# Optimization experiments

Measured on AMD Instinct MI355X. Metric: run time of the kernel, lower is better.

Reference implementation:

```python
import jax, jax.numpy as jnp
import numpy as np

B, L, A, D, H = 128, 48, 16, 256, 128
NEG = 1e10


def l2norm(v, eps=1e-8):
    return v / (jnp.sqrt(jnp.sum(v * v, axis=-1, keepdims=True)) + eps)


def setup_inputs():
    key = jax.random.key(0)
    ks = jax.random.split(key, 6)
    x = jax.random.normal(ks[0], (B, L, A, D), jnp.float32)
    lengths = jax.random.randint(ks[1], (B,), 8, L + 1)
    lengths = lengths.at[0].set(L)  # forward assumes lengths.max() == L
    audio_masks = (jax.random.uniform(ks[2], (B, L, A, 1)) < 0.7).astype(jnp.float32)
    audio_masks = audio_masks.at[..., 0, :].set(1.0)  # at least one valid frame per word
    w_sem = jax.random.normal(ks[3], (D, D), jnp.float32) * 0.05   # Linear(D,D,bias=False).weight
    w1 = jax.random.normal(ks[4], (H, 2 * D), jnp.float32) * 0.05  # Linear(2D,H).weight
    b1 = jnp.zeros((H,), jnp.float32)
    w2 = jax.random.normal(ks[5], (1, H), jnp.float32) * 0.05      # Linear(H,1,bias=False).weight
    return {"x": x, "lengths": lengths, "audio_masks": audio_masks,
            "w_sem": w_sem, "w1": w1, "b1": b1, "w2": w2}


def _merge(arr, cv, idx):
    """update_with_mask with fixed-length arrays: new[j]=arr[j] (j<idx), cv (j==idx), arr[j+1] (j>idx).
    Trailing garbage slot is masked downstream by length masks."""
    shift = jnp.concatenate([arr[:, 1:], arr[:, -1:]], axis=1)
    extra = (1,) * (arr.ndim - 2)
    j = jnp.arange(arr.shape[1]).reshape((1, -1) + extra)
    ib = idx.reshape((-1, 1) + extra)
    return jnp.where(j < ib, arr, jnp.where(j == ib, jnp.expand_dims(cv, 1), shift))


def _forward(x, lengths, audio_masks, w_sem, w1, b1, w2):
    Bq, Lq = x.shape[0], x.shape[1]
    S = Lq - 1  # max_select_cnt (lengths.max() == Lq)
    # masked max over audio frames: [B,L,D]
    sem0 = jnp.max(jnp.einsum('blad,ed->blae', x, w_sem) - NEG * (1.0 - audio_masks), axis=-2)
    word_mask = (jnp.arange(Lq)[None, :] < lengths[:, None]).astype(x.dtype)
    out_word = sem0 * word_mask[..., None]
    pos = jnp.arange(Lq, dtype=jnp.int32)
    bounds0 = jnp.broadcast_to(pos, (Bq, Lq))
    posm1 = jnp.arange(Lq - 1)

    def gat(a, k):  # gather along axis 1 at per-batch index
        return jnp.take_along_axis(a, k.reshape((-1, 1) + (1,) * (a.ndim - 2)), axis=1)[:, 0]

    def step(carry, i):
        syn, sem, lb, rb = carry
        valid = jnp.clip(lengths - 1 - i, 0)               # merges still allowed per sentence
        masked = (posm1[None, :] >= valid[:, None]).astype(x.dtype)
        undone = (valid > 0).astype(x.dtype)[:, None]
        feats = jnp.concatenate([l2norm(syn[:, 1:]), l2norm(syn[:, :-1])], axis=-1)  # [B,L-1,2D]
        h = jax.nn.relu(jnp.einsum('bld,hd->blh', feats, w1) + b1)
        logits = jnp.einsum('blh,oh->blo', h, w2)[..., 0] - NEG * masked
        probs = jax.nn.softmax(logits, axis=1)
        idx = jnp.argmax(probs, axis=1).astype(jnp.int32)  # volatile=True (greedy) path
        tp = jnp.take_along_axis(probs, idx[:, None], axis=1)[:, 0]
        s_l, s_r = gat(sem, idx), gat(sem, idx + 1)
        feat = l2norm(s_l + s_r)
        spans = jnp.stack([gat(lb, idx), gat(rb, idx + 1)], axis=1)  # [B,2]
        syn_c = l2norm(gat(syn, idx) + gat(syn, idx + 1))
        carry = (_merge(syn, syn_c, idx), _merge(sem, feat, idx),
                 _merge(lb, spans[:, 0], idx), _merge(rb, spans[:, 1], idx))
        outs = (feat * undone, l2norm(s_l) * undone, l2norm(s_r) * undone, idx, tp, spans)
        return carry, outs

    _, (features, lefts, rights, tree_idx, tree_probs, span_bounds) = jax.lax.scan(
        step, (sem0, sem0, bounds0, bounds0), jnp.arange(S))
    return features, lefts, rights, out_word, tree_idx, tree_probs, span_bounds


def reference(x, lengths, audio_masks, w_sem, w1, b1, w2):
    return _forward(x, lengths, audio_masks, w_sem, w1, b1, w2)
```

## Files before the change

kernel.cpp:

```cpp
#include <hip/hip_runtime.h>
#include <math.h>

#define NEGC 1e10f
#define EPSF 1e-8f

#define NB 128
#define NL 48
#define NA 16
#define ND 256
#define NH 128
#define NS 47
#define PB_STRIDE (NL*ND)

#define WS_WT   0
#define WS_INVN 65536
#define WS_LOG  (65536+6144)
#define WS_PHYS (65536+12288)

#define O_FEAT  0
#define O_LEFT  1540096
#define O_RIGHT 3080192
#define O_WORD  4620288
#define O_TIDX  6193152
#define O_TP    6199168
#define O_SPAN  6205184

__device__ __forceinline__ void ldsbar() {
  asm volatile("s_waitcnt lgkmcnt(0)" ::: "memory");
  __builtin_amdgcn_s_barrier();
  __builtin_amdgcn_sched_barrier(0);
}

__global__ __launch_bounds__(256) void k_transpose(const float* __restrict__ w_sem,
                                                   float* __restrict__ ws) {
  int blk = blockIdx.x, t = threadIdx.x;
  ws[WS_WT + blk*256 + t] = w_sem[t*256 + blk];
}

__global__ __launch_bounds__(128) void k_sem0(const float* __restrict__ x,
                                              const int* __restrict__ lengths,
                                              const float* __restrict__ amask,
                                              float* __restrict__ ws,
                                              float* __restrict__ out) {
  __shared__ float xs[2*NA*128];
  __shared__ float pen[2*NA];
  int bl0 = blockIdx.x * 2;
  int t = threadIdx.x;
  int wv = t >> 6;
  int c = t & 63;
  int bl = bl0 + wv;
  int b = bl / NL, l = bl - b*NL;
  int l0 = bl0 % NL;
  int lenB = lengths[bl0 / NL];
  int e0 = c*4;

  if (l0 >= lenB) {
    float4 z = make_float4(0.f, 0.f, 0.f, 0.f);
    *(float4*)(ws + WS_PHYS + (size_t)b*PB_STRIDE + l*ND + e0) = z;
    *(float4*)(out + O_WORD + (size_t)bl*ND + e0) = z;
    if (c == 0) ws[WS_INVN + bl] = 1.0f / (sqrtf(0.f) + EPSF);
    return;
  }
  bool live  = (l < lenB);
  bool live1 = (l0 + 1 < lenB);

  if (t < 2*NA) pen[t] = -NEGC * (1.0f - amask[(size_t)(bl0 + (t >> 4))*NA + (t & 15)]);
  float4* xs4 = (float4*)xs;
  const float* wt = ws + WS_WT;
  float acc[NA][4];
#pragma unroll
  for (int a = 0; a < NA; ++a) { acc[a][0]=0.f; acc[a][1]=0.f; acc[a][2]=0.f; acc[a][3]=0.f; }
  bool va[NA];

  for (int p = 0; p < 2; ++p) {
    if (p) __syncthreads();
#pragma unroll
    for (int r = 0; r < 8; ++r) {
      int f = t + 128*r;
      int tile = f >> 9, rem = f & 511;
      int a = rem >> 5, dq = rem & 31;
      if (tile == 0 || live1) {
        const float4* xg4 = (const float4*)(x + (size_t)(bl0 + tile)*(NA*ND));
        xs4[f] = xg4[a*64 + p*32 + dq];
      }
    }
    __syncthreads();
    if (p == 0) {
#pragma unroll
      for (int a = 0; a < NA; ++a) va[a] = live && (pen[wv*NA + a] == 0.0f);
    }
    if (live) {
      for (int d0 = 0; d0 < 128; d0 += 4) {
        const float* wrow = wt + (size_t)(p*128 + d0)*ND + e0;
        float4 wr0 = *(const float4*)(wrow);
        float4 wr1 = *(const float4*)(wrow + ND);
        float4 wr2 = *(const float4*)(wrow + 2*ND);
        float4 wr3 = *(const float4*)(wrow + 3*ND);
#pragma unroll
        for (int a = 0; a < NA; ++a) {
          if (va[a]) {
            float4 xa = xs4[wv*512 + a*32 + (d0 >> 2)];
            acc[a][0] = fmaf(xa.x, wr0.x, acc[a][0]);
            acc[a][1] = fmaf(xa.x, wr0.y, acc[a][1]);
            acc[a][2] = fmaf(xa.x, wr0.z, acc[a][2]);
            acc[a][3] = fmaf(xa.x, wr0.w, acc[a][3]);
            acc[a][0] = fmaf(xa.y, wr1.x, acc[a][0]);
            acc[a][1] = fmaf(xa.y, wr1.y, acc[a][1]);
            acc[a][2] = fmaf(xa.y, wr1.z, acc[a][2]);
            acc[a][3] = fmaf(xa.y, wr1.w, acc[a][3]);
            acc[a][0] = fmaf(xa.z, wr2.x, acc[a][0]);
            acc[a][1] = fmaf(xa.z, wr2.y, acc[a][1]);
            acc[a][2] = fmaf(xa.z, wr2.z, acc[a][2]);
            acc[a][3] = fmaf(xa.z, wr2.w, acc[a][3]);
            acc[a][0] = fmaf(xa.w, wr3.x, acc[a][0]);
            acc[a][1] = fmaf(xa.w, wr3.y, acc[a][1]);
            acc[a][2] = fmaf(xa.w, wr3.z, acc[a][2]);
            acc[a][3] = fmaf(xa.w, wr3.w, acc[a][3]);
          }
        }
      }
    }
  }
  float m0 = -INFINITY, m1 = -INFINITY, m2 = -INFINITY, m3 = -INFINITY;
#pragma unroll
  for (int a = 0; a < NA; ++a) {
    if (va[a]) {
      m0 = fmaxf(m0, acc[a][0]);
      m1 = fmaxf(m1, acc[a][1]);
      m2 = fmaxf(m2, acc[a][2]);
      m3 = fmaxf(m3, acc[a][3]);
    }
  }
  if (!live) { m0 = 0.f; m1 = 0.f; m2 = 0.f; m3 = 0.f; }
  float* prow = ws + WS_PHYS + (size_t)b*PB_STRIDE + l*ND;
  *(float4*)(prow + e0) = make_float4(m0, m1, m2, m3);
  float wm = live ? 1.0f : 0.0f;
  *(float4*)(out + O_WORD + (size_t)bl*ND + e0) = make_float4(m0*wm, m1*wm, m2*wm, m3*wm);
  float s2 = m0*m0 + m1*m1 + m2*m2 + m3*m3;
#pragma unroll
  for (int off = 32; off; off >>= 1) s2 += __shfl_down(s2, off);
  if (c == 0) ws[WS_INVN + bl] = 1.0f / (sqrtf(s2) + EPSF);
}

__global__ __launch_bounds__(512, 1) void k_prelogits(float* __restrict__ ws,
                                                      const int* __restrict__ lengths,
                                                      const float* __restrict__ w1g,
                                                      const float* __restrict__ b1g,
                                                      const float* __restrict__ w2g) {
  __shared__ float rows[25*ND];
  __shared__ float part[4*8*NH];
  __shared__ float invl[25];
  __shared__ float b1s[NH];
  __shared__ float w2s[NH];
  int bid = blockIdx.x;
  int b = bid >> 1, h = bid & 1;
  int p0 = h*24;
  int np = h ? 23 : 24;
  int nrows = h ? 24 : 25;
  int t = threadIdx.x;
  int lane = t & 63, wv = t >> 6;
  int j = t & 127, q = t >> 7;

  int lenB = lengths[b];
  int npl = lenB - 1 - p0;
  if (npl > np) npl = np;
  if (npl <= 0) return;

  float w1f[128];
  {
    const float4* wsrc = (const float4*)(w1g + (size_t)j*512 + q*128);
#pragma unroll
    for (int kk = 0; kk < 32; ++kk) {
      float4 v = wsrc[kk];
      w1f[4*kk+0] = v.x; w1f[4*kk+1] = v.y; w1f[4*kk+2] = v.z; w1f[4*kk+3] = v.w;
    }
  }
#pragma unroll
  for (int kk = 0; kk < 32; ++kk)
    asm volatile("" : "+v"(w1f[4*kk+0]), "+v"(w1f[4*kk+1]), "+v"(w1f[4*kk+2]), "+v"(w1f[4*kk+3]));

  if (t < NH) { b1s[t] = b1g[t]; w2s[t] = w2g[t]; }
  if (t < nrows) invl[t] = ws[WS_INVN + b*48 + p0 + t];
  {
    const float4* pg4 = (const float4*)(ws + WS_PHYS + (size_t)b*PB_STRIDE);
    float4* rows4 = (float4*)rows;
    int n4 = nrows * 64;
    for (int u = t; u < n4; u += 512) rows4[u] = pg4[p0*64 + u];
  }
  __syncthreads();

  for (int ct = 0; ct < 3; ++ct) {
    if (ct*8 >= npl) break;
#pragma unroll
    for (int c = 0; c < 8; ++c) {
      int pp = ct*8 + c;
      if (pp < npl) {
        int rloc = (q < 2) ? pp + 1 : pp;
        const float4* rp4 = (const float4*)(rows + rloc*ND + (q & 1)*128);
        float ax = 0.f, ay = 0.f, az = 0.f, aw = 0.f;
#pragma unroll
        for (int kk = 0; kk < 32; ++kk) {
          float4 rv = rp4[kk];
          ax = fmaf(w1f[4*kk+0], rv.x, ax);
          ay = fmaf(w1f[4*kk+1], rv.y, ay);
          az = fmaf(w1f[4*kk+2], rv.z, az);
          aw = fmaf(w1f[4*kk+3], rv.w, aw);
        }
        part[(q*8 + c)*NH + j] = (ax + ay) + (az + aw);
      }
    }
    __syncthreads();
    int pp = ct*8 + wv;
    if (pp < npl) {
      float inR = invl[pp + 1], inL = invl[pp];
      float pr0 = part[(0*8+wv)*NH + lane]      + part[(1*8+wv)*NH + lane];
      float pl0 = part[(2*8+wv)*NH + lane]      + part[(3*8+wv)*NH + lane];
      float pr1 = part[(0*8+wv)*NH + lane + 64] + part[(1*8+wv)*NH + lane + 64];
      float pl1 = part[(2*8+wv)*NH + lane + 64] + part[(3*8+wv)*NH + lane + 64];
      float h0 = fmaf(inR, pr0, fmaf(inL, pl0, b1s[lane]));
      float h1 = fmaf(inR, pr1, fmaf(inL, pl1, b1s[lane + 64]));
      h0 = fmaxf(h0, 0.f); h1 = fmaxf(h1, 0.f);
      float v = w2s[lane]*h0 + w2s[lane + 64]*h1;
#pragma unroll
      for (int off = 32; off; off >>= 1) v += __shfl_down(v, off);
      if (lane == 0) ws[WS_LOG + b*48 + p0 + pp] = v;
    }
    __syncthreads();
  }
}

__global__ __launch_bounds__(1024, 1) void k_tree(const int* __restrict__ lengths,
                                                  float* __restrict__ ws,
                                                  const float* __restrict__ w1g,
                                                  const float* __restrict__ b1g,
                                                  const float* __restrict__ w2g,
                                                  float* __restrict__ out) {
  __shared__ float rows[NL*ND];
  __shared__ float part[16*NH];
  __shared__ float logits[48];
  __shared__ int physIdx[48];
  __shared__ int lbA[48];
  __shared__ int rbA[48];
  __shared__ float invn[48];
  __shared__ float b1s[NH];
  __shared__ float w2s[NH];
  __shared__ float red[8];
  __shared__ int s_idx, s_rL;
  __shared__ float s_tp, s_max;

  int b = blockIdx.x;
  int t = threadIdx.x;
  int lane = t & 63, wv = t >> 6;
  int j = t & 127, s8 = t >> 7;
  int len = lengths[b];

  float w1f[64];
  {
    const float4* wsrc = (const float4*)(w1g + (size_t)j*512 + s8*64);
#pragma unroll
    for (int kk = 0; kk < 16; ++kk) {
      float4 v = wsrc[kk];
      w1f[4*kk+0] = v.x; w1f[4*kk+1] = v.y; w1f[4*kk+2] = v.z; w1f[4*kk+3] = v.w;
    }
  }
#pragma unroll
  for (int kk = 0; kk < 16; ++kk)
    asm volatile("" : "+v"(w1f[4*kk+0]), "+v"(w1f[4*kk+1]), "+v"(w1f[4*kk+2]), "+v"(w1f[4*kk+3]));

  if (t < NH) { b1s[t] = b1g[t]; w2s[t] = w2g[t]; }
  if (t < 48) { physIdx[t] = t; lbA[t] = t; rbA[t] = t; invn[t] = ws[WS_INVN + b*48 + t]; }
  if (t < 47) logits[t] = ws[WS_LOG + b*48 + t];
  {
    const float4* pg4 = (const float4*)(ws + WS_PHYS + (size_t)b*PB_STRIDE);
    float4* rows4 = (float4*)rows;
    for (int u = t; u < NL*64; u += 1024) rows4[u] = pg4[u];
  }
  __syncthreads();

  auto gemv_pos = [&](int pos, int slot) {
    int r = (s8 < 4) ? physIdx[pos + 1] : physIdx[pos];
    const float4* rp4 = (const float4*)(rows + r*ND + (s8 & 3)*64);
    float ax = 0.f, ay = 0.f, az = 0.f, aw = 0.f;
#pragma unroll
    for (int kk = 0; kk < 16; ++kk) {
      float4 rv = rp4[kk];
      ax = fmaf(w1f[4*kk+0], rv.x, ax);
      ay = fmaf(w1f[4*kk+1], rv.y, ay);
      az = fmaf(w1f[4*kk+2], rv.z, az);
      aw = fmaf(w1f[4*kk+3], rv.w, aw);
    }
    part[(s8*2 + slot)*NH + j] = (ax + ay) + (az + aw);
  };

  int pidx = -1;
  for (int i = 0; i < NS; ++i) {
    int valid = len - 1 - i; if (valid < 0) valid = 0;
    if (i > 0 && t == 0)
      invn[s_rL] = 1.0f / (sqrtf(red[4]+red[5]+red[6]+red[7]) + EPSF);
    if (valid >= 2) {
      if (i > 0) {
        int pos0 = -1, pos1 = -1, np = 0;
        if (pidx > 0) { pos0 = pidx - 1; np = 1; }
        if (pidx <= valid - 1) { if (np) pos1 = pidx; else pos0 = pidx; ++np; }
        gemv_pos(pos0, 0);
        if (np > 1) gemv_pos(pos1, 1);
        ldsbar();
        if (wv < np) {
          int p = (wv == 0) ? pos0 : pos1;
          int rR = physIdx[p + 1], rLL = physIdx[p];
          float inR = invn[rR], inL = invn[rLL];
          float pr0 = (part[(0*2+wv)*NH + lane]      + part[(1*2+wv)*NH + lane])
                    + (part[(2*2+wv)*NH + lane]      + part[(3*2+wv)*NH + lane]);
          float pl0 = (part[(4*2+wv)*NH + lane]      + part[(5*2+wv)*NH + lane])
                    + (part[(6*2+wv)*NH + lane]      + part[(7*2+wv)*NH + lane]);
          float pr1 = (part[(0*2+wv)*NH + lane + 64] + part[(1*2+wv)*NH + lane + 64])
                    + (part[(2*2+wv)*NH + lane + 64] + part[(3*2+wv)*NH + lane + 64]);
          float pl1 = (part[(4*2+wv)*NH + lane + 64] + part[(5*2+wv)*NH + lane + 64])
                    + (part[(6*2+wv)*NH + lane + 64] + part[(7*2+wv)*NH + lane + 64]);
          float h0 = fmaf(inR, pr0, fmaf(inL, pl0, b1s[lane]));
          float h1 = fmaf(inR, pr1, fmaf(inL, pl1, b1s[lane + 64]));
          h0 = fmaxf(h0, 0.f); h1 = fmaxf(h1, 0.f);
          float v = w2s[lane]*h0 + w2s[lane + 64]*h1;
#pragma unroll
          for (int off = 32; off; off >>= 1) v += __shfl_down(v, off);
          if (lane == 0) logits[p] = v;
        }
        ldsbar();
      }
      if (wv == 0) {
        float v = (lane < valid) ? logits[lane] : -INFINITY;
        int bi = lane;
#pragma unroll
        for (int off = 32; off; off >>= 1) {
          float ov = __shfl_down(v, off);
          int  oi = __shfl_down(bi, off);
          if (ov > v || (ov == v && oi < bi)) { v = ov; bi = oi; }
        }
        if (lane == 0) { s_idx = bi; s_max = v; }
      }
    } else {
      if (t == 0) { s_idx = 0; s_tp = (valid == 1) ? 1.0f : (1.0f/47.0f); }
    }
    ldsbar();
    int idx = s_idx;
    int rL = 0, rR = 0; float slv = 0.f, srv = 0.f, inL = 0.f, inR = 0.f, sumv = 0.f;
    if (t < ND) {
      rL = physIdx[idx]; rR = physIdx[idx + 1];
      slv = rows[rL*ND + t]; srv = rows[rR*ND + t];
      inL = invn[rL]; inR = invn[rR];
      sumv = slv + srv;
      float q2 = sumv * sumv;
#pragma unroll
      for (int off = 32; off; off >>= 1) q2 += __shfl_down(q2, off);
      if (lane == 0) red[wv] = q2;
    }
    int sp0 = 0, sp1 = 0;
    if (t == 0) { s_rL = rL; sp0 = lbA[idx]; sp1 = rbA[idx + 1]; }
    if (wv == 4 && valid >= 2) {
      float ee = (lane < valid) ? expf(logits[lane] - s_max) : 0.f;
#pragma unroll
      for (int off = 32; off; off >>= 1) ee += __shfl_down(ee, off);
      if (lane == 0) s_tp = 1.0f / ee;
    }
    int tt = t - 320;
    int pv = 0, lv = 0, rv_ = 0; float gv = 0.f;
    if (wv == 5 && tt < 47) { pv = physIdx[tt+1]; lv = lbA[tt+1]; rv_ = rbA[tt+1]; gv = logits[tt+1]; }
    ldsbar();
    float undone = valid > 0 ? 1.0f : 0.0f;
    if (t < ND) {
      float invns = 1.0f / (sqrtf(red[0]+red[1]+red[2]+red[3]) + EPSF);
      float featv = sumv * invns;
      int ob = (i*NB + b)*ND + t;
      out[O_FEAT  + ob] = featv * undone;
      out[O_LEFT  + ob] = slv * inL * undone;
      out[O_RIGHT + ob] = srv * inR * undone;
      rows[rL*ND + t] = featv;
      float q3 = featv * featv;
#pragma unroll
      for (int off = 32; off; off >>= 1) q3 += __shfl_down(q3, off);
      if (lane == 0) red[4 + wv] = q3;
    }
    if (t == 0) {
      out[O_TIDX + i*NB + b] = (float)idx;
      out[O_TP   + i*NB + b] = s_tp;
      out[O_SPAN + (i*NB + b)*2 + 0] = (float)sp0;
      out[O_SPAN + (i*NB + b)*2 + 1] = (float)sp1;
    }
    if (wv == 5 && tt < 47) {
      if (tt > idx) { physIdx[tt] = pv; lbA[tt] = lv; logits[tt] = gv; }
      if (tt >= idx) rbA[tt] = rv_;
    }
    ldsbar();
    pidx = idx;
  }
}

extern "C" void kernel_launch(void* const* d_in, const int* in_sizes, int n_in,
                              void* d_out, int out_size, void* d_ws, size_t ws_size,
                              hipStream_t stream) {
  const float* x      = (const float*)d_in[0];
  const int*   lengths= (const int*)  d_in[1];
  const float* amask  = (const float*)d_in[2];
  const float* w_sem  = (const float*)d_in[3];
  const float* w1     = (const float*)d_in[4];
  const float* b1     = (const float*)d_in[5];
  const float* w2     = (const float*)d_in[6];
  float* out = (float*)d_out;
  float* ws  = (float*)d_ws;

  k_transpose<<<dim3(256), dim3(256), 0, stream>>>(w_sem, ws);
  k_sem0<<<dim3(NB*NL/2), dim3(128), 0, stream>>>(x, lengths, amask, ws, out);
  k_prelogits<<<dim3(256), dim3(512), 0, stream>>>(ws, lengths, w1, b1, w2);
  k_tree<<<dim3(NB), dim3(1024), 0, stream>>>(lengths, ws, w1, b1, w2, out);
}
```

Before: 326.9 us.

## Prefetch weight rows in sem0 and fuse logit finish with argmax in one wave

In the sem0 projection kernel, the next four transposed-weight rows are loaded into registers with inline asm while the current rows feed the FMAs, and a launch-bounds occupancy hint is added. The goal is to hide global load latency in the inner loop. In the sequential tree loop, wave 0 now computes both updated logits and runs the argmax directly from registers. This removes one LDS barrier and a round trip through shared memory per step. The trade-offs are extra register pressure from double-buffered weights and less wave parallelism in the logit computation.

Result: slower. 373.2 us (+14.2%).

```diff
diff --git a/kernel.cpp b/kernel.cpp
--- a/kernel.cpp
+++ b/kernel.cpp
@@ -31,17 +31,19 @@
   __builtin_amdgcn_sched_barrier(0);
 }
 
+#define GLOAD4(dst, addr) asm volatile("global_load_dwordx4 %0, %1, off" : "=v"(dst) : "v"(addr))
+
 __global__ __launch_bounds__(256) void k_transpose(const float* __restrict__ w_sem,
                                                    float* __restrict__ ws) {
   int blk = blockIdx.x, t = threadIdx.x;
   ws[WS_WT + blk*256 + t] = w_sem[t*256 + blk];
 }
 
-__global__ __launch_bounds__(128) void k_sem0(const float* __restrict__ x,
-                                              const int* __restrict__ lengths,
-                                              const float* __restrict__ amask,
-                                              float* __restrict__ ws,
-                                              float* __restrict__ out) {
+__global__ __launch_bounds__(128, 4) void k_sem0(const float* __restrict__ x,
+                                                 const int* __restrict__ lengths,
+                                                 const float* __restrict__ amask,
+                                                 float* __restrict__ ws,
+                                                 float* __restrict__ out) {
   __shared__ float xs[2*NA*128];
   __shared__ float pen[2*NA];
   int bl0 = blockIdx.x * 2;
@@ -72,6 +74,15 @@
   for (int a = 0; a < NA; ++a) { acc[a][0]=0.f; acc[a][1]=0.f; acc[a][2]=0.f; acc[a][3]=0.f; }
   bool va[NA];
 
+  float4 cw0, cw1, cw2, cw3, nw0, nw1, nw2, nw3;
+  {
+    const float* wr = wt + e0;
+    cw0 = *(const float4*)(wr);
+    cw1 = *(const float4*)(wr + ND);
+    cw2 = *(const float4*)(wr + 2*ND);
+    cw3 = *(const float4*)(wr + 3*ND);
+  }
+
   for (int p = 0; p < 2; ++p) {
     if (p) __syncthreads();
 #pragma unroll
@@ -91,32 +102,41 @@
     }
     if (live) {
       for (int d0 = 0; d0 < 128; d0 += 4) {
-        const float* wrow = wt + (size_t)(p*128 + d0)*ND + e0;
-        float4 wr0 = *(const float4*)(wrow);
-        float4 wr1 = *(const float4*)(wrow + ND);
-        float4 wr2 = *(const float4*)(wrow + 2*ND);
-        float4 wr3 = *(const float4*)(wrow + 3*ND);
+        int g = p*128 + d0;
+        bool pf = (g < 252);
+        if (pf) {
+          const float* wr = wt + (size_t)(g + 4)*ND + e0;
+          GLOAD4(nw0, wr);
+          GLOAD4(nw1, wr + ND);
+          GLOAD4(nw2, wr + 2*ND);
+          GLOAD4(nw3, wr + 3*ND);
+        }
 #pragma unroll
         for (int a = 0; a < NA; ++a) {
           if (va[a]) {
             float4 xa = xs4[wv*512 + a*32 + (d0 >> 2)];
-            acc[a][0] = fmaf(xa.x, wr0.x, acc[a][0]);
-            acc[a][1] = fmaf(xa.x, wr0.y, acc[a][1]);
-            acc[a][2] = fmaf(xa.x, wr0.z, acc[a][2]);
-            acc[a][3] = fmaf(xa.x, wr0.w, acc[a][3]);
-            acc[a][0] = fmaf(xa.y, wr1.x, acc[a][0]);
-            acc[a][1] = fmaf(xa.y, wr1.y, acc[a][1]);
-            acc[a][2] = fmaf(xa.y, wr1.z, acc[a][2]);
-            acc[a][3] = fmaf(xa.y, wr1.w, acc[a][3]);
-            acc[a][0] = fmaf(xa.z, wr2.x, acc[a][0]);
-            acc[a][1] = fmaf(xa.z, wr2.y, acc[a][1]);
-            acc[a][2] = fmaf(xa.z, wr2.z, acc[a][2]);
-            acc[a][3] = fmaf(xa.z, wr2.w, acc[a][3]);
-            acc[a][0] = fmaf(xa.w, wr3.x, acc[a][0]);
-            acc[a][1] = fmaf(xa.w, wr3.y, acc[a][1]);
-            acc[a][2] = fmaf(xa.w, wr3.z, acc[a][2]);
-            acc[a][3] = fmaf(xa.w, wr3.w, acc[a][3]);
+            acc[a][0] = fmaf(xa.x, cw0.x, acc[a][0]);
+            acc[a][1] = fmaf(xa.x, cw0.y, acc[a][1]);
+            acc[a][2] = fmaf(xa.x, cw0.z, acc[a][2]);
+            acc[a][3] = fmaf(xa.x, cw0.w, acc[a][3]);
+            acc[a][0] = fmaf(xa.y, cw1.x, acc[a][0]);
+            acc[a][1] = fmaf(xa.y, cw1.y, acc[a][1]);
+            acc[a][2] = fmaf(xa.y, cw1.z, acc[a][2]);
+            acc[a][3] = fmaf(xa.y, cw1.w, acc[a][3]);
+            acc[a][0] = fmaf(xa.z, cw2.x, acc[a][0]);
+            acc[a][1] = fmaf(xa.z, cw2.y, acc[a][1]);
+            acc[a][2] = fmaf(xa.z, cw2.z, acc[a][2]);
+            acc[a][3] = fmaf(xa.z, cw2.w, acc[a][3]);
+            acc[a][0] = fmaf(xa.w, cw3.x, acc[a][0]);
+            acc[a][1] = fmaf(xa.w, cw3.y, acc[a][1]);
+            acc[a][2] = fmaf(xa.w, cw3.z, acc[a][2]);
+            acc[a][3] = fmaf(xa.w, cw3.w, acc[a][3]);
           }
+        }
+        if (pf) {
+          asm volatile("s_waitcnt vmcnt(0)" ::: "memory");
+          __builtin_amdgcn_sched_barrier(0);
+          cw0 = nw0; cw1 = nw1; cw2 = nw2; cw3 = nw3;
         }
       }
     }
@@ -305,38 +325,68 @@
         gemv_pos(pos0, 0);
         if (np > 1) gemv_pos(pos1, 1);
         ldsbar();
-        if (wv < np) {
-          int p = (wv == 0) ? pos0 : pos1;
-          int rR = physIdx[p + 1], rLL = physIdx[p];
-          float inR = invn[rR], inL = invn[rLL];
-          float pr0 = (part[(0*2+wv)*NH + lane]      + part[(1*2+wv)*NH + lane])
-                    + (part[(2*2+wv)*NH + lane]      + part[(3*2+wv)*NH + lane]);
-          float pl0 = (part[(4*2+wv)*NH + lane]      + part[(5*2+wv)*NH + lane])
-                    + (part[(6*2+wv)*NH + lane]      + part[(7*2+wv)*NH + lane]);
-          float pr1 = (part[(0*2+wv)*NH + lane + 64] + part[(1*2+wv)*NH + lane + 64])
-                    + (part[(2*2+wv)*NH + lane + 64] + part[(3*2+wv)*NH + lane + 64]);
-          float pl1 = (part[(4*2+wv)*NH + lane + 64] + part[(5*2+wv)*NH + lane + 64])
-                    + (part[(6*2+wv)*NH + lane + 64] + part[(7*2+wv)*NH + lane + 64]);
-          float h0 = fmaf(inR, pr0, fmaf(inL, pl0, b1s[lane]));
-          float h1 = fmaf(inR, pr1, fmaf(inL, pl1, b1s[lane + 64]));
+        if (wv == 0) {
+          float inR0 = invn[physIdx[pos0 + 1]], inL0 = invn[physIdx[pos0]];
+          float pr0 = (part[(0*2+0)*NH + lane]      + part[(1*2+0)*NH + lane])
+                    + (part[(2*2+0)*NH + lane]      + part[(3*2+0)*NH + lane]);
+          float pl0 = (part[(4*2+0)*NH + lane]      + part[(5*2+0)*NH + lane])
+                    + (part[(6*2+0)*NH + lane]      + part[(7*2+0)*NH + lane]);
+          float pr1 = (part[(0*2+0)*NH + lane + 64] + part[(1*2+0)*NH + lane + 64])
+                    + (part[(2*2+0)*NH + lane + 64] + part[(3*2+0)*NH + lane + 64]);
+          float pl1 = (part[(4*2+0)*NH + lane + 64] + part[(5*2+0)*NH + lane + 64])
+                    + (part[(6*2+0)*NH + lane + 64] + part[(7*2+0)*NH + lane + 64]);
+          float h0 = fmaf(inR0, pr0, fmaf(inL0, pl0, b1s[lane]));
+          float h1 = fmaf(inR0, pr1, fmaf(inL0, pl1, b1s[lane + 64]));
           h0 = fmaxf(h0, 0.f); h1 = fmaxf(h1, 0.f);
-          float v = w2s[lane]*h0 + w2s[lane + 64]*h1;
-#pragma unroll
-          for (int off = 32; off; off >>= 1) v += __shfl_down(v, off);
-          if (lane == 0) logits[p] = v;
-        }
-        ldsbar();
-      }
-      if (wv == 0) {
-        float v = (lane < valid) ? logits[lane] : -INFINITY;
-        int bi = lane;
-#pragma unroll
-        for (int off = 32; off; off >>= 1) {
-          float ov = __shfl_down(v, off);
-          int  oi = __shfl_down(bi, off);
-          if (ov > v || (ov == v && oi < bi)) { v = ov; bi = oi; }
-        }
-        if (lane == 0) { s_idx = bi; s_max = v; }
+          float v0 = w2s[lane]*h0 + w2s[lane + 64]*h1;
+          float v1 = 0.f;
+          if (np > 1) {
+            float inR1 = invn[physIdx[pos1 + 1]], inL1 = invn[physIdx[pos1]];
+            float qr0 = (part[(0*2+1)*NH + lane]      + part[(1*2+1)*NH + lane])
+                      + (part[(2*2+1)*NH + lane]      + part[(3*2+1)*NH + lane]);
+            float ql0 = (part[(4*2+1)*NH + lane]      + part[(5*2+1)*NH + lane])
+                      + (part[(6*2+1)*NH + lane]      + part[(7*2+1)*NH + lane]);
+            float qr1 = (part[(0*2+1)*NH + lane + 64] + part[(1*2+1)*NH + lane + 64])
+                      + (part[(2*2+1)*NH + lane + 64] + part[(3*2+1)*NH + lane + 64]);
+            float ql1 = (part[(4*2+1)*NH + lane + 64] + part[(5*2+1)*NH + lane + 64])
+                      + (part[(6*2+1)*NH + lane + 64] + part[(7*2+1)*NH + lane + 64]);
+            float g0 = fmaf(inR1, qr0, fmaf(inL1, ql0, b1s[lane]));
+            float g1 = fmaf(inR1, qr1, fmaf(inL1, ql1, b1s[lane + 64]));
+            g0 = fmaxf(g0, 0.f); g1 = fmaxf(g1, 0.f);
+            v1 = w2s[lane]*g0 + w2s[lane + 64]*g1;
+          }
+#pragma unroll
+          for (int off = 32; off; off >>= 1) { v0 += __shfl_down(v0, off); v1 += __shfl_down(v1, off); }
+          float fresh0 = __shfl(v0, 0);
+          float fresh1 = __shfl(v1, 0);
+          float ev = (lane < valid) ? logits[lane] : -INFINITY;
+          if (lane == pos0) ev = fresh0;
+          if (np > 1 && lane == pos1) ev = fresh1;
+          float v = ev; int bi = lane;
+#pragma unroll
+          for (int off = 32; off; off >>= 1) {
+            float ov = __shfl_down(v, off);
+            int  oi = __shfl_down(bi, off);
+            if (ov > v || (ov == v && oi < bi)) { v = ov; bi = oi; }
+          }
+          if (lane == 0) {
+            s_idx = bi; s_max = v;
+            logits[pos0] = fresh0;
+            if (np > 1) logits[pos1] = fresh1;
+          }
+        }
+      } else {
+        if (wv == 0) {
+          float v = (lane < valid) ? logits[lane] : -INFINITY;
+          int bi = lane;
+#pragma unroll
+          for (int off = 32; off; off >>= 1) {
+            float ov = __shfl_down(v, off);
+            int  oi = __shfl_down(bi, off);
+            if (ov > v || (ov == v && oi < bi)) { v = ov; bi = oi; }
+          }
+          if (lane == 0) { s_idx = bi; s_max = v; }
+        }
       }
     } else {
       if (t == 0) { s_idx = 0; s_tp = (valid == 1) ? 1.0f : (1.0f/47.0f); }
```
